# Optimization experiments

Hardware: AMD Instinct MI355X
Metric: run time of the kernel (lower is better)

## Reference

```python
import jax, jax.numpy as jnp
import numpy as np

L, B, T, D, H, A, F, V, BIAS_DIM, E = 6, 16, 512, 512, 8, 64, 2048, 10000, 4, 200000
LN_EPS = 1e-3  # keras LayerNormalization default


def positional_encoding(d, max_len):
    pos = np.arange(max_len, dtype=np.float32)[:, None]
    i = np.arange(d, dtype=np.float32)[None, :]
    angle = pos / np.power(10000.0, (2.0 * np.floor(i / 2.0)) / d)
    pe = np.where((np.arange(d) % 2) == 0, np.sin(angle), np.cos(angle))
    return jnp.asarray(pe, jnp.float32)


def layer_norm(x, g, b):
    mu = jnp.mean(x, -1, keepdims=True)
    var = jnp.mean(jnp.square(x - mu), -1, keepdims=True)
    return (x - mu) * jax.lax.rsqrt(var + LN_EPS) * g + b


def attention(x, masks, bias_idx, Wq, Wk, Wv, Wo, be, bs):
    q = jnp.einsum('btd,dha->btha', x, Wq)
    k = jnp.einsum('btd,dha->btha', x, Wk)
    v = jnp.einsum('btd,dha->btha', x, Wv)
    alpha = jnp.einsum('bkha,bqha->bhqk', k, q)
    # sparse edge bias: scalar per edge = bias_embs[type] @ bias_scalar
    ev = (be[bias_idx[:, 0]] @ bs)[:, 0]                      # [E]
    dense = jnp.zeros((x.shape[0], x.shape[1], x.shape[1]), x.dtype)
    dense = dense.at[bias_idx[:, 1], bias_idx[:, 2], bias_idx[:, 3]].add(ev)  # scatter_nd semantics (add)
    ksum = jnp.sum(k, -1)                                     # [B,T,H]
    alpha = alpha + jnp.einsum('bqk,bkh->bhqk', dense, ksum)
    alpha = alpha * jax.lax.rsqrt(jnp.float32(A))
    alpha = alpha * masks + (1.0 - jnp.ceil(masks)) * jnp.finfo(jnp.float32).min
    alpha = jax.nn.softmax(alpha, -1)
    ctx = jnp.einsum('bhqk,bkha->bqha', alpha, v)
    return jnp.einsum('btha,had->btd', ctx, Wo)


def setup_inputs() -> dict:
    key = jax.random.key(0)
    ks = jax.random.split(key, 24)
    tokens = jax.random.randint(ks[0], (B, T), 0, V, dtype=jnp.int32)
    masks = jnp.ones((B, 1, T, T), jnp.float32)
    ab = jnp.stack([
        jax.random.randint(ks[1], (E,), 0, BIAS_DIM, dtype=jnp.int32),
        jax.random.randint(ks[2], (E,), 0, B, dtype=jnp.int32),
        jax.random.randint(ks[3], (E,), 0, T, dtype=jnp.int32),
        jax.random.randint(ks[4], (E,), 0, T, dtype=jnp.int32)], axis=1)
    s = 0.03
    return {
        'tokens': tokens, 'masks': masks, 'attention_bias': ab,
        'embed': jax.random.normal(ks[5], (V, D)) * (D ** -0.5),
        'Wq': jax.random.normal(ks[6], (L, D, H, A)) * s,
        'Wk': jax.random.normal(ks[7], (L, D, H, A)) * s,
        'Wv': jax.random.normal(ks[8], (L, D, H, A)) * s,
        'Wo': jax.random.normal(ks[9], (L, H, A, D)) * s,
        'be': jax.random.normal(ks[10], (L, BIAS_DIM, A)) * s,
        'bs': jax.random.normal(ks[11], (L, A, 1)) * s,
        'ln_g': jnp.ones((L, 2, D)), 'ln_b': jnp.zeros((L, 2, D)),
        'ff1_w': jax.random.normal(ks[12], (L, D, F)) * s,
        'ff1_b': jnp.zeros((L, F)),
        'ff2_w': jax.random.normal(ks[13], (L, F, D)) * s,
        'ff2_b': jnp.zeros((L, D)),
        'lnout_g': jnp.ones((D,)), 'lnout_b': jnp.zeros((D,)),
    }


def reference(tokens, masks, attention_bias, embed, Wq, Wk, Wv, Wo, be, bs,
              ln_g, ln_b, ff1_w, ff1_b, ff2_w, ff2_b, lnout_g, lnout_b):
    pos_enc = positional_encoding(D, 5000)
    x = embed[tokens] * jnp.sqrt(jnp.float32(D)) + pos_enc[:T]
    for l in range(L):
        h = layer_norm(x, ln_g[l, 0], ln_b[l, 0])
        x = x + attention(h, masks, attention_bias, Wq[l], Wk[l], Wv[l], Wo[l], be[l], bs[l])
        h = layer_norm(x, ln_g[l, 1], ln_b[l, 1])
        x = x + jax.nn.relu(h @ ff1_w[l] + ff1_b[l]) @ ff2_w[l] + ff2_b[l]
    return layer_norm(x, lnout_g, lnout_b)
```

## Files before the change

kernel.cpp:

```cpp
#include <hip/hip_runtime.h>
#include <hip/hip_bf16.h>

#define LNUM 6
#define BB 16
#define TT 512
#define DD 512
#define HH 8
#define AA 64
#define FFD 2048
#define EE 200000
#define BIASDIM 4
#define ATT_NEG (-3.402823466e38f)

typedef __bf16 bf16_t;
typedef __attribute__((ext_vector_type(8))) __bf16 bf16x8;
typedef __attribute__((ext_vector_type(4))) float f32x4;

typedef __attribute__((address_space(3))) void lds_void;
typedef const __attribute__((address_space(1))) void glb_void;

__device__ __forceinline__ void async_load16(const bf16_t* g, bf16_t* l) {
    __builtin_amdgcn_global_load_lds((glb_void*)g, (lds_void*)l, 16, 0, 0);
}

__global__ __launch_bounds__(256) void embed_pe_kernel(
    const int* __restrict__ tokens, const float* __restrict__ embed,
    float* __restrict__ x)
{
    int idx = blockIdx.x * 256 + threadIdx.x;
    int d  = idx & (DD - 1);
    int bt = idx >> 9;
    int t  = bt & (TT - 1);
    int tok = tokens[bt];
    float e = embed[(long long)tok * DD + d] * 22.62741699796952f;
    float p = (float)(2 * (d >> 1)) * (1.0f / (float)DD);
    float denom = exp2f(p * 13.287712379549449f);
    float angle = (float)t / denom;
    float pe = (d & 1) ? cosf(angle) : sinf(angle);
    x[idx] = e + pe;
}

template <typename TO>
__global__ __launch_bounds__(256) void ln_kernel(
    const float* __restrict__ x, TO* __restrict__ y,
    const float* __restrict__ g, const float* __restrict__ b)
{
    long long row = blockIdx.x;
    const float* xr = x + row * DD;
    int tid = threadIdx.x;
    float v0 = xr[tid], v1 = xr[tid + 256];
    float s = v0 + v1, sq = v0 * v0 + v1 * v1;
#pragma unroll
    for (int o = 32; o > 0; o >>= 1) {
        s  += __shfl_down(s, o);
        sq += __shfl_down(sq, o);
    }
    __shared__ float ss[4], sq4[4];
    if ((tid & 63) == 0) { ss[tid >> 6] = s; sq4[tid >> 6] = sq; }
    __syncthreads();
    float st  = ss[0] + ss[1] + ss[2] + ss[3];
    float sqt = sq4[0] + sq4[1] + sq4[2] + sq4[3];
    float mean = st * (1.0f / DD);
    float var  = sqt * (1.0f / DD) - mean * mean;
    float inv  = rsqrtf(var + 1e-3f);
    y[row * DD + tid]       = (TO)((v0 - mean) * inv * g[tid]       + b[tid]);
    y[row * DD + tid + 256] = (TO)((v1 - mean) * inv * g[tid + 256] + b[tid + 256]);
}

__global__ __launch_bounds__(256) void ksum_kernel(
    const bf16_t* __restrict__ k, float* __restrict__ ks)
{
    int idx = blockIdx.x * 256 + threadIdx.x;
    long long base = (long long)idx * AA;
    float s = 0.f;
#pragma unroll
    for (int a = 0; a < AA; a++) s += (float)k[base + a];
    ks[idx] = s;
}

__global__ __launch_bounds__(256) void bias_scatter_kernel(
    const int* __restrict__ ab, const float* __restrict__ be,
    const float* __restrict__ bs, float* __restrict__ dense)
{
    __shared__ float ev[BIASDIM];
    int tid = threadIdx.x;
    if (tid < BIASDIM) {
        float s = 0.f;
        for (int a = 0; a < AA; a++) s += be[tid * AA + a] * bs[a];
        ev[tid] = s;
    }
    __syncthreads();
    int e = blockIdx.x * 256 + tid;
    if (e < EE) {
        int ty = ab[e * 4 + 0];
        int b  = ab[e * 4 + 1];
        int q  = ab[e * 4 + 2];
        int kk = ab[e * 4 + 3];
        atomicAdd(&dense[((long long)b * TT + q) * TT + kk], ev[ty]);
    }
}

__global__ __launch_bounds__(256) void wconv_kernel(
    const float* __restrict__ in, bf16_t* __restrict__ out, int R, int Cc)
{
    __shared__ bf16_t tile[64][65];
    int c0 = blockIdx.x * 64, r0 = blockIdx.y * 64;
    int tid = threadIdx.x;
#pragma unroll
    for (int i = 0; i < 16; i++) {
        int idx = tid + i * 256; int r = idx >> 6, c = idx & 63;
        tile[c][r] = (bf16_t)in[(long long)(r0 + r) * Cc + c0 + c];
    }
    __syncthreads();
#pragma unroll
    for (int i = 0; i < 16; i++) {
        int idx = tid + i * 256; int rr = idx >> 6, cc = idx & 63;
        out[(long long)(c0 + rr) * R + r0 + cc] = tile[rr][cc];
    }
}

struct Ptr4 { const float* p[4]; };

__global__ __launch_bounds__(256) void wconv4_kernel(Ptr4 srcs, bf16_t* __restrict__ out)
{
    __shared__ bf16_t tile[64][65];
    int z = blockIdx.z;
    const float* in = srcs.p[z];
    bf16_t* o = out + (long long)z * DD * DD;
    int c0 = blockIdx.x * 64, r0 = blockIdx.y * 64;
    int tid = threadIdx.x;
#pragma unroll
    for (int i = 0; i < 16; i++) {
        int idx = tid + i * 256; int r = idx >> 6, c = idx & 63;
        tile[c][r] = (bf16_t)in[(long long)(r0 + r) * DD + c0 + c];
    }
    __syncthreads();
#pragma unroll
    for (int i = 0; i < 16; i++) {
        int idx = tid + i * 256; int rr = idx >> 6, cc = idx & 63;
        o[(long long)(c0 + rr) * DD + r0 + cc] = tile[rr][cc];
    }
}

__global__ __launch_bounds__(256) void vtrans_kernel(
    const bf16_t* __restrict__ v, bf16_t* __restrict__ vT)
{
    __shared__ bf16_t tile[64][65];
    int bh = blockIdx.y; int b = bh >> 3, h = bh & 7;
    int t0 = blockIdx.x * 64;
    int tid = threadIdx.x;
#pragma unroll
    for (int i = 0; i < 16; i++) {
        int idx = tid + i * 256; int r = idx >> 6, c = idx & 63;
        tile[c][r] = v[((long long)(b * TT + t0 + r) * HH + h) * AA + c];
    }
    __syncthreads();
#pragma unroll
    for (int i = 0; i < 16; i++) {
        int idx = tid + i * 256; int a = idx >> 6, t2 = idx & 63;
        vT[(((long long)b * HH + h) * AA + a) * TT + t0 + t2] = tile[a][t2];
    }
}

__global__ __launch_bounds__(256) void fused_attn_kernel(
    const bf16_t* __restrict__ qg, const bf16_t* __restrict__ kg,
    const bf16_t* __restrict__ vT, const float* __restrict__ dense,
    const float* __restrict__ ksum, const float* __restrict__ masks,
    bf16_t* __restrict__ ctx)
{
    __shared__ __align__(16) bf16_t Ks[64 * 64];
    __shared__ __align__(16) bf16_t Vs[64 * 64];
    __shared__ __align__(16) bf16_t Plds[4 * 16 * 88];

    int tid = threadIdx.x;
    int wave = tid >> 6, lane = tid & 63;
    int row16 = lane & 15, quad = lane >> 4;
    int bh = blockIdx.y; int b = bh >> 3, h = bh & 7;
    int qw = blockIdx.x * 64 + wave * 16;

    bf16x8 qf[2];
    {
        const bf16_t* qp = qg + (((long long)b * TT + qw + row16) * HH + h) * AA + quad * 8;
        qf[0] = *(const bf16x8*)(qp);
        qf[1] = *(const bf16x8*)(qp + 32);
    }

    f32x4 o[4] = {};
    float m_r[4], l_r[4];
#pragma unroll
    for (int r = 0; r < 4; r++) { m_r[r] = -3.0e38f; l_r[r] = 0.f; }

    bf16_t* Pw = Plds + wave * 16 * 88;
    const float* dbase = dense + (long long)b * TT * TT;
    const float* mbase = masks + (long long)b * TT * TT;

    for (int kt = 0; kt < 8; kt++) {
        int t0 = kt * 64;
#pragma unroll
        for (int p = tid; p < 512; p += 256) {
            int r = p >> 3, s = p & 7, c = s ^ (r & 7);
            async_load16(kg + (((long long)b * TT + t0 + r) * HH + h) * AA + c * 8,
                         Ks + p * 8);
        }
#pragma unroll
        for (int p = tid; p < 512; p += 256) {
            int r = p >> 3, s = p & 7, c = s ^ (r & 7);
            async_load16(vT + ((long long)bh * AA + r) * TT + t0 + c * 8,
                         Vs + p * 8);
        }
        __syncthreads();

        f32x4 s4[4] = {};
#pragma unroll
        for (int n = 0; n < 4; n++) {
            int row = n * 16 + row16;
            int sw = row & 7;
            bf16x8 kf0 = *(const bf16x8*)(Ks + row * 64 + ((quad ^ sw) * 8));
            bf16x8 kf1 = *(const bf16x8*)(Ks + row * 64 + (((quad + 4) ^ sw) * 8));
            s4[n] = __builtin_amdgcn_mfma_f32_16x16x32_bf16(qf[0], kf0, s4[n], 0, 0, 0);
            s4[n] = __builtin_amdgcn_mfma_f32_16x16x32_bf16(qf[1], kf1, s4[n], 0, 0, 0);
        }

        float val[4][4];
#pragma unroll
        for (int n = 0; n < 4; n++) {
            int ktok = t0 + n * 16 + row16;
            float ksv = ksum[((long long)b * TT + ktok) * HH + h];
#pragma unroll
            for (int r = 0; r < 4; r++) {
                int qgl = qw + quad * 4 + r;
                float d  = dbase[(long long)qgl * TT + ktok];
                float mk = mbase[(long long)qgl * TT + ktok];
                float vv = 0.125f * fmaf(d, ksv, s4[n][r]);
                val[n][r] = vv * mk + (1.0f - ceilf(mk)) * ATT_NEG;
            }
        }

        float scl[4];
#pragma unroll
        for (int r = 0; r < 4; r++) {
            float mx = fmaxf(fmaxf(val[0][r], val[1][r]), fmaxf(val[2][r], val[3][r]));
#pragma unroll
            for (int off = 1; off < 16; off <<= 1) mx = fmaxf(mx, __shfl_xor(mx, off));
            float mnew = fmaxf(m_r[r], mx);
            float sc = __expf(m_r[r] - mnew);
            float ps = 0.f;
#pragma unroll
            for (int n = 0; n < 4; n++) {
                float p = __expf(val[n][r] - mnew);
                val[n][r] = p;
                ps += p;
            }
#pragma unroll
            for (int off = 1; off < 16; off <<= 1) ps += __shfl_xor(ps, off);
            l_r[r] = l_r[r] * sc + ps;
            m_r[r] = mnew;
            scl[r] = sc;
        }
#pragma unroll
        for (int j = 0; j < 4; j++)
#pragma unroll
            for (int r = 0; r < 4; r++) o[j][r] *= scl[r];

#pragma unroll
        for (int n = 0; n < 4; n++)
#pragma unroll
            for (int r = 0; r < 4; r++)
                Pw[(quad * 4 + r) * 88 + n * 16 + row16] = (bf16_t)val[n][r];
        asm volatile("s_waitcnt lgkmcnt(0)" ::: "memory");

        bf16x8 pa0 = *(const bf16x8*)(Pw + row16 * 88 + quad * 8);
        bf16x8 pa1 = *(const bf16x8*)(Pw + row16 * 88 + 32 + quad * 8);
#pragma unroll
        for (int j = 0; j < 4; j++) {
            int row = j * 16 + row16;
            int sw = row & 7;
            bf16x8 vb0 = *(const bf16x8*)(Vs + row * 64 + ((quad ^ sw) * 8));
            bf16x8 vb1 = *(const bf16x8*)(Vs + row * 64 + (((quad + 4) ^ sw) * 8));
            o[j] = __builtin_amdgcn_mfma_f32_16x16x32_bf16(pa0, vb0, o[j], 0, 0, 0);
            o[j] = __builtin_amdgcn_mfma_f32_16x16x32_bf16(pa1, vb1, o[j], 0, 0, 0);
        }
        __syncthreads();
    }

#pragma unroll
    for (int r = 0; r < 4; r++) {
        float invl = 1.0f / l_r[r];
        int qgl = qw + quad * 4 + r;
        bf16_t* cp = ctx + (((long long)b * TT + qgl) * HH + h) * AA;
#pragma unroll
        for (int j = 0; j < 4; j++)
            cp[j * 16 + row16] = (bf16_t)(o[j][r] * invl);
    }
}

template <int BM, int BN, typename TC>
__global__ __launch_bounds__((BM / 64) * (BN / 64) * 64) void gemm_mfma(
    const bf16_t* __restrict__ Ag, const bf16_t* __restrict__ Bg, TC* __restrict__ Cg,
    int K, int lda, int ldb, int ldc,
    long long sAz, long long sBz, long long sCz,
    const float* __restrict__ bias, int accum, int relu)
{
    constexpr int WN = BN / 64;
    constexpr int NT = (BM / 64) * (BN / 64) * 64;
    __shared__ __align__(16) bf16_t As[2][BM * 32];
    __shared__ __align__(16) bf16_t Bs[2][BN * 32];

    int z = blockIdx.z;
    Ag += z * sAz; Bg += z * sBz; Cg += z * sCz;

    int tid = threadIdx.x;
    int wave = tid >> 6, lane = tid & 63;
    int wm = (wave / WN) * 64, wn = (wave % WN) * 64;
    int m0 = blockIdx.x * BM, n0 = blockIdx.y * BN;
    int row16 = lane & 15, quad = lane >> 4;

    f32x4 acc[4][4] = {};

#pragma unroll
    for (int p = tid; p < BM * 4; p += NT) {
        int r = p >> 2, c = p & 3;
        async_load16(Ag + (long long)(m0 + r) * lda + c * 8, As[0] + p * 8);
    }
#pragma unroll
    for (int p = tid; p < BN * 4; p += NT) {
        int r = p >> 2, c = p & 3;
        async_load16(Bg + (long long)(n0 + r) * ldb + c * 8, Bs[0] + p * 8);
    }

    int ib = 0;
    for (int k0 = 0; k0 < K; k0 += 32, ib ^= 1) {
        __syncthreads();
        if (k0 + 32 < K) {
            int kn = k0 + 32;
#pragma unroll
            for (int p = tid; p < BM * 4; p += NT) {
                int r = p >> 2, c = p & 3;
                async_load16(Ag + (long long)(m0 + r) * lda + kn + c * 8,
                             As[ib ^ 1] + p * 8);
            }
#pragma unroll
            for (int p = tid; p < BN * 4; p += NT) {
                int r = p >> 2, c = p & 3;
                async_load16(Bg + (long long)(n0 + r) * ldb + kn + c * 8,
                             Bs[ib ^ 1] + p * 8);
            }
        }
        bf16x8 af[4], bfr[4];
#pragma unroll
        for (int i = 0; i < 4; i++)
            af[i] = *(const bf16x8*)(As[ib] + (wm + i * 16 + row16) * 32 + quad * 8);
#pragma unroll
        for (int j = 0; j < 4; j++)
            bfr[j] = *(const bf16x8*)(Bs[ib] + (wn + j * 16 + row16) * 32 + quad * 8);
#pragma unroll
        for (int i = 0; i < 4; i++)
#pragma unroll
            for (int j = 0; j < 4; j++)
                acc[i][j] = __builtin_amdgcn_mfma_f32_16x16x32_bf16(
                    af[i], bfr[j], acc[i][j], 0, 0, 0);
    }

#pragma unroll
    for (int i = 0; i < 4; i++) {
#pragma unroll
        for (int j = 0; j < 4; j++) {
#pragma unroll
            for (int r = 0; r < 4; r++) {
                int m = m0 + wm + i * 16 + quad * 4 + r;
                int n = n0 + wn + j * 16 + row16;
                float vv = acc[i][j][r];
                if (bias) vv += bias[n];
                if (accum) vv += (float)Cg[(long long)m * ldc + n];
                if (relu) vv = fmaxf(vv, 0.f);
                Cg[(long long)m * ldc + n] = (TC)vv;
            }
        }
    }
}

extern "C" void kernel_launch(void* const* d_in, const int* in_sizes, int n_in,
                              void* d_out, int out_size, void* d_ws, size_t ws_size,
                              hipStream_t stream)
{
    const int*   tokens = (const int*)d_in[0];
    const float* masks  = (const float*)d_in[1];
    const int*   ab     = (const int*)d_in[2];
    const float* embed  = (const float*)d_in[3];
    const float* Wq     = (const float*)d_in[4];
    const float* Wk     = (const float*)d_in[5];
    const float* Wv     = (const float*)d_in[6];
    const float* Wo     = (const float*)d_in[7];
    const float* be     = (const float*)d_in[8];
    const float* bs     = (const float*)d_in[9];
    const float* ln_g   = (const float*)d_in[10];
    const float* ln_b   = (const float*)d_in[11];
    const float* ff1w   = (const float*)d_in[12];
    const float* ff1b   = (const float*)d_in[13];
    const float* ff2w   = (const float*)d_in[14];
    const float* ff2b   = (const float*)d_in[15];
    const float* lng    = (const float*)d_in[16];
    const float* lnb    = (const float*)d_in[17];
    float* out = (float*)d_out;

    const long long NX = (long long)BB * TT * DD;
    float* x     = (float*)d_ws;
    float* dense = x + NX;
    float* ks    = dense + (long long)BB * TT * TT;
    bf16_t* h_bf = (bf16_t*)(ks + (long long)BB * TT * HH);
    bf16_t* q    = h_bf + NX;
    bf16_t* k    = q + NX;
    bf16_t* v    = k + NX;
    bf16_t* vT   = v + NX;
    bf16_t* wqT  = vT + NX;
    bf16_t* wkT  = wqT + (long long)DD * DD;
    bf16_t* wvT  = wkT + (long long)DD * DD;
    bf16_t* woT  = wvT + (long long)DD * DD;
    bf16_t* ff1T = woT + (long long)DD * DD;
    bf16_t* ff2T = ff1T + (long long)DD * FFD;
    bf16_t* ffm  = ff2T + (long long)FFD * DD;

    embed_pe_kernel<<<dim3(NX / 256), dim3(256), 0, stream>>>(tokens, embed, x);

    for (int l = 0; l < LNUM; l++) {
        Ptr4 p4;
        p4.p[0] = Wq + (long long)l * DD * HH * AA;
        p4.p[1] = Wk + (long long)l * DD * HH * AA;
        p4.p[2] = Wv + (long long)l * DD * HH * AA;
        p4.p[3] = Wo + (long long)l * HH * AA * DD;
        wconv4_kernel<<<dim3(8, 8, 4), dim3(256), 0, stream>>>(p4, wqT);
        wconv_kernel<<<dim3(FFD / 64, DD / 64, 1), dim3(256), 0, stream>>>(
            ff1w + (long long)l * DD * FFD, ff1T, DD, FFD);
        wconv_kernel<<<dim3(DD / 64, FFD / 64, 1), dim3(256), 0, stream>>>(
            ff2w + (long long)l * FFD * DD, ff2T, FFD, DD);

        const float* ff1b_l = ff1b + (long long)l * FFD;
        const float* ff2b_l = ff2b + (long long)l * DD;

        ln_kernel<bf16_t><<<dim3(BB * TT), dim3(256), 0, stream>>>(
            x, h_bf, ln_g + (l * 2 + 0) * DD, ln_b + (l * 2 + 0) * DD);

        gemm_mfma<128, 128, bf16_t><<<dim3(64, 4, 3), dim3(256), 0, stream>>>(
            h_bf, wqT, q, 512, 512, 512, 512,
            0LL, (long long)DD * DD, NX, nullptr, 0, 0);

        vtrans_kernel<<<dim3(8, BB * HH), dim3(256), 0, stream>>>(v, vT);
        ksum_kernel<<<dim3(BB * TT * HH / 256), dim3(256), 0, stream>>>(k, ks);

        hipMemsetAsync(dense, 0, sizeof(float) * (size_t)BB * TT * TT, stream);
        bias_scatter_kernel<<<dim3((EE + 255) / 256), dim3(256), 0, stream>>>(
            ab, be + (long long)l * BIASDIM * AA, bs + (long long)l * AA, dense);

        fused_attn_kernel<<<dim3(TT / 64, BB * HH), dim3(256), 0, stream>>>(
            q, k, vT, dense, ks, masks, h_bf);

        gemm_mfma<128, 64, float><<<dim3(64, 8, 1), dim3(128), 0, stream>>>(
            h_bf, woT, x, 512, 512, 512, 512,
            0LL, 0LL, 0LL, nullptr, 1, 0);

        ln_kernel<bf16_t><<<dim3(BB * TT), dim3(256), 0, stream>>>(
            x, h_bf, ln_g + (l * 2 + 1) * DD, ln_b + (l * 2 + 1) * DD);

        gemm_mfma<128, 128, bf16_t><<<dim3(64, 16, 1), dim3(256), 0, stream>>>(
            h_bf, ff1T, ffm, 512, 512, 512, 2048, 0LL, 0LL, 0LL, ff1b_l, 0, 1);

        gemm_mfma<128, 64, float><<<dim3(64, 8, 1), dim3(128), 0, stream>>>(
            ffm, ff2T, x, 2048, 2048, 2048, 512,
            0LL, 0LL, 0LL, ff2b_l, 1, 0);
    }

    ln_kernel<float><<<dim3(BB * TT), dim3(256), 0, stream>>>(x, out, lng, lnb);
}
```

Before: 1.733 ms.

## Split-K the Wo and FF2 GEMMs and fuse partial reduction into LayerNorm

The Wo projection and FF2 GEMMs (N=512, so only 512 tiles) now use split-K across 2 and 4 slices to put more blocks on the GPU. Slice 0 adds directly into the residual, and the other slices write fp32 partials into the reused dense-bias buffer. A new reduce_ln kernel sums those partials into x and applies the next LayerNorm in one pass. This replaces the separate LN launches but adds extra fp32 partial traffic, and the buffer reuse depends on the ordering of later memset and scatter writes.

After: 1.705 ms. Within noise of the previous version (-1.6%).

```diff
diff --git a/kernel.cpp b/kernel.cpp
--- a/kernel.cpp
+++ b/kernel.cpp
@@ -67,6 +67,40 @@
     y[row * DD + tid + 256] = (TO)((v1 - mean) * inv * g[tid + 256] + b[tid + 256]);
 }
 
+template <typename TO, int S>
+__global__ __launch_bounds__(256) void reduce_ln_kernel(
+    float* __restrict__ x, const float* __restrict__ P,
+    TO* __restrict__ y, const float* __restrict__ g, const float* __restrict__ b)
+{
+    const long long NXc = (long long)BB * TT * DD;
+    long long row = blockIdx.x;
+    int tid = threadIdx.x;
+    long long i0 = row * DD + tid;
+    float v0 = x[i0], v1 = x[i0 + 256];
+#pragma unroll
+    for (int s = 0; s < S; s++) {
+        v0 += P[(long long)s * NXc + i0];
+        v1 += P[(long long)s * NXc + i0 + 256];
+    }
+    x[i0] = v0; x[i0 + 256] = v1;
+    float s2 = v0 + v1, sq = v0 * v0 + v1 * v1;
+#pragma unroll
+    for (int o = 32; o > 0; o >>= 1) {
+        s2 += __shfl_down(s2, o);
+        sq += __shfl_down(sq, o);
+    }
+    __shared__ float ss[4], sq4[4];
+    if ((tid & 63) == 0) { ss[tid >> 6] = s2; sq4[tid >> 6] = sq; }
+    __syncthreads();
+    float st  = ss[0] + ss[1] + ss[2] + ss[3];
+    float sqt = sq4[0] + sq4[1] + sq4[2] + sq4[3];
+    float mean = st * (1.0f / DD);
+    float var  = sqt * (1.0f / DD) - mean * mean;
+    float inv  = rsqrtf(var + 1e-3f);
+    y[i0]       = (TO)((v0 - mean) * inv * g[tid]       + b[tid]);
+    y[i0 + 256] = (TO)((v1 - mean) * inv * g[tid + 256] + b[tid + 256]);
+}
+
 __global__ __launch_bounds__(256) void ksum_kernel(
     const bf16_t* __restrict__ k, float* __restrict__ ks)
 {
@@ -374,6 +408,95 @@
                 if (accum) vv += (float)Cg[(long long)m * ldc + n];
                 if (relu) vv = fmaxf(vv, 0.f);
                 Cg[(long long)m * ldc + n] = (TC)vv;
+            }
+        }
+    }
+}
+
+template <int BM, int BN, int SPLIT>
+__global__ __launch_bounds__((BM / 64) * (BN / 64) * 64) void gemm_splitk(
+    const bf16_t* __restrict__ Ag, const bf16_t* __restrict__ Bg,
+    float* __restrict__ Cg, float* __restrict__ Pg,
+    int K, int lda, int ldb, int ldc, const float* __restrict__ bias)
+{
+    constexpr int WN = BN / 64;
+    constexpr int NT = (BM / 64) * (BN / 64) * 64;
+    __shared__ __align__(16) bf16_t As[2][BM * 32];
+    __shared__ __align__(16) bf16_t Bs[2][BN * 32];
+
+    int z = blockIdx.z;
+    int kc = K / SPLIT;
+    int kbeg = z * kc, kend = kbeg + kc;
+
+    int tid = threadIdx.x;
+    int wave = tid >> 6, lane = tid & 63;
+    int wm = (wave / WN) * 64, wn = (wave % WN) * 64;
+    int m0 = blockIdx.x * BM, n0 = blockIdx.y * BN;
+    int row16 = lane & 15, quad = lane >> 4;
+
+    f32x4 acc[4][4] = {};
+
+#pragma unroll
+    for (int p = tid; p < BM * 4; p += NT) {
+        int r = p >> 2, c = p & 3;
+        async_load16(Ag + (long long)(m0 + r) * lda + kbeg + c * 8, As[0] + p * 8);
+    }
+#pragma unroll
+    for (int p = tid; p < BN * 4; p += NT) {
+        int r = p >> 2, c = p & 3;
+        async_load16(Bg + (long long)(n0 + r) * ldb + kbeg + c * 8, Bs[0] + p * 8);
+    }
+
+    int ib = 0;
+    for (int k0 = kbeg; k0 < kend; k0 += 32, ib ^= 1) {
+        __syncthreads();
+        if (k0 + 32 < kend) {
+            int kn = k0 + 32;
+#pragma unroll
+            for (int p = tid; p < BM * 4; p += NT) {
+                int r = p >> 2, c = p & 3;
+                async_load16(Ag + (long long)(m0 + r) * lda + kn + c * 8,
+                             As[ib ^ 1] + p * 8);
+            }
+#pragma unroll
+            for (int p = tid; p < BN * 4; p += NT) {
+                int r = p >> 2, c = p & 3;
+                async_load16(Bg + (long long)(n0 + r) * ldb + kn + c * 8,
+                             Bs[ib ^ 1] + p * 8);
+            }
+        }
+        bf16x8 af[4], bfr[4];
+#pragma unroll
+        for (int i = 0; i < 4; i++)
+            af[i] = *(const bf16x8*)(As[ib] + (wm + i * 16 + row16) * 32 + quad * 8);
+#pragma unroll
+        for (int j = 0; j < 4; j++)
+            bfr[j] = *(const bf16x8*)(Bs[ib] + (wn + j * 16 + row16) * 32 + quad * 8);
+#pragma unroll
+        for (int i = 0; i < 4; i++)
+#pragma unroll
+            for (int j = 0; j < 4; j++)
+                acc[i][j] = __builtin_amdgcn_mfma_f32_16x16x32_bf16(
+                    af[i], bfr[j], acc[i][j], 0, 0, 0);
+    }
+
+    const long long NXc = (long long)BB * TT * DD;
+#pragma unroll
+    for (int i = 0; i < 4; i++) {
+#pragma unroll
+        for (int j = 0; j < 4; j++) {
+#pragma unroll
+            for (int r = 0; r < 4; r++) {
+                int m = m0 + wm + i * 16 + quad * 4 + r;
+                int n = n0 + wn + j * 16 + row16;
+                float vv = acc[i][j][r];
+                if (z == 0) {
+                    if (bias) vv += bias[n];
+                    long long ci = (long long)m * ldc + n;
+                    Cg[ci] = Cg[ci] + vv;
+                } else {
+                    Pg[(long long)(z - 1) * NXc + (long long)m * ldc + n] = vv;
+                }
             }
         }
     }
@@ -405,10 +528,10 @@
 
     const long long NX = (long long)BB * TT * DD;
     float* x     = (float*)d_ws;
-    float* dense = x + NX;
-    float* ks    = dense + (long long)BB * TT * TT;
+    float* ks    = x + NX;
     bf16_t* h_bf = (bf16_t*)(ks + (long long)BB * TT * HH);
-    bf16_t* q    = h_bf + NX;
+    float* dense = (float*)(h_bf + NX);
+    bf16_t* q    = (bf16_t*)(dense + (long long)BB * TT * TT);
     bf16_t* k    = q + NX;
     bf16_t* v    = k + NX;
     bf16_t* vT   = v + NX;
@@ -420,9 +543,20 @@
     bf16_t* ff2T = ff1T + (long long)DD * FFD;
     bf16_t* ffm  = ff2T + (long long)FFD * DD;
 
+    float* partCtx = dense;
+    float* partFF  = dense;
+
     embed_pe_kernel<<<dim3(NX / 256), dim3(256), 0, stream>>>(tokens, embed, x);
 
     for (int l = 0; l < LNUM; l++) {
+        if (l == 0) {
+            ln_kernel<bf16_t><<<dim3(BB * TT), dim3(256), 0, stream>>>(
+                x, h_bf, ln_g + (l * 2 + 0) * DD, ln_b + (l * 2 + 0) * DD);
+        } else {
+            reduce_ln_kernel<bf16_t, 3><<<dim3(BB * TT), dim3(256), 0, stream>>>(
+                x, partFF, h_bf, ln_g + (l * 2 + 0) * DD, ln_b + (l * 2 + 0) * DD);
+        }
+
         Ptr4 p4;
         p4.p[0] = Wq + (long long)l * DD * HH * AA;
         p4.p[1] = Wk + (long long)l * DD * HH * AA;
@@ -437,9 +571,6 @@
         const float* ff1b_l = ff1b + (long long)l * FFD;
         const float* ff2b_l = ff2b + (long long)l * DD;
 
-        ln_kernel<bf16_t><<<dim3(BB * TT), dim3(256), 0, stream>>>(
-            x, h_bf, ln_g + (l * 2 + 0) * DD, ln_b + (l * 2 + 0) * DD);
-
         gemm_mfma<128, 128, bf16_t><<<dim3(64, 4, 3), dim3(256), 0, stream>>>(
             h_bf, wqT, q, 512, 512, 512, 512,
             0LL, (long long)DD * DD, NX, nullptr, 0, 0);
@@ -454,20 +585,19 @@
         fused_attn_kernel<<<dim3(TT / 64, BB * HH), dim3(256), 0, stream>>>(
             q, k, vT, dense, ks, masks, h_bf);
 
-        gemm_mfma<128, 64, float><<<dim3(64, 8, 1), dim3(128), 0, stream>>>(
-            h_bf, woT, x, 512, 512, 512, 512,
-            0LL, 0LL, 0LL, nullptr, 1, 0);
-
-        ln_kernel<bf16_t><<<dim3(BB * TT), dim3(256), 0, stream>>>(
-            x, h_bf, ln_g + (l * 2 + 1) * DD, ln_b + (l * 2 + 1) * DD);
+        gemm_splitk<128, 64, 2><<<dim3(64, 8, 2), dim3(128), 0, stream>>>(
+            h_bf, woT, x, partCtx, 512, 512, 512, 512, nullptr);
+
+        reduce_ln_kernel<bf16_t, 1><<<dim3(BB * TT), dim3(256), 0, stream>>>(
+            x, partCtx, h_bf, ln_g + (l * 2 + 1) * DD, ln_b + (l * 2 + 1) * DD);
 
         gemm_mfma<128, 128, bf16_t><<<dim3(64, 16, 1), dim3(256), 0, stream>>>(
             h_bf, ff1T, ffm, 512, 512, 512, 2048, 0LL, 0LL, 0LL, ff1b_l, 0, 1);
 
-        gemm_mfma<128, 64, float><<<dim3(64, 8, 1), dim3(128), 0, stream>>>(
-            ffm, ff2T, x, 2048, 2048, 2048, 512,
-            0LL, 0LL, 0LL, ff2b_l, 1, 0);
-    }
-
-    ln_kernel<float><<<dim3(BB * TT), dim3(256), 0, stream>>>(x, out, lng, lnb);
-}
+        gemm_splitk<128, 64, 4><<<dim3(64, 8, 4), dim3(128), 0, stream>>>(
+            ffm, ff2T, x, partFF, 2048, 2048, 2048, 512, ff2b_l);
+    }
+
+    reduce_ln_kernel<float, 3><<<dim3(BB * TT), dim3(256), 0, stream>>>(
+        x, partFF, out, lng, lnb);
+}
```
